# Performance work log

Measured on AMD Instinct MI355X. Metric: run time of the kernel, lower is better.

The kernel has to match this reference:

```python
import jax, jax.numpy as jnp
import numpy as np

B, S, D = 2, 2048, 768
E, L = 4, 2
H = 4 * D  # dim_mlp = dim * mlp_ratio
EPS = 1e-6


def setup_inputs() -> dict:
    key = jax.random.key(0)
    ks = jax.random.split(key, 4)
    x = jax.random.normal(ks[0], (B, S, D), dtype=jnp.float32)
    expert_idx = jax.random.randint(ks[1], (B, S), 0, E, dtype=jnp.int32)
    # Linear weights: normal(std=0.02), biases zero (per init_weights).
    W1 = 0.02 * jax.random.normal(ks[2], (L, E, D, H), dtype=jnp.float32)
    b1 = jnp.zeros((L, E, H), dtype=jnp.float32)
    W2 = 0.02 * jax.random.normal(ks[3], (L, E, H, D), dtype=jnp.float32)
    b2 = jnp.zeros((L, E, D), dtype=jnp.float32)
    # LayerNorm: weight=1, bias=0 (per init_weights).
    ln_g = jnp.ones((L, D), dtype=jnp.float32)
    ln_b = jnp.zeros((L, D), dtype=jnp.float32)
    return {"x": x, "expert_idx": expert_idx, "W1": W1, "b1": b1,
            "W2": W2, "b2": b2, "ln_g": ln_g, "ln_b": ln_b}


def _layernorm(x, g, b):
    mu = jnp.mean(x, axis=-1, keepdims=True)
    var = jnp.mean(jnp.square(x - mu), axis=-1, keepdims=True)
    return (x - mu) * jax.lax.rsqrt(var + EPS) * g + b


def reference(x, expert_idx, W1, b1, W2, b2, ln_g, ln_b):
    # Eval mode: Dropout and DropPath are identity.
    idx = expert_idx[:, :, None, None]  # [B,S,1,1] for gather over expert axis
    for i in range(L):
        h = _layernorm(x, ln_g[i], ln_b[i])                       # [B,S,D]
        # All experts' FFNs computed densely (as in the torch module).
        a = jnp.einsum('bsd,edh->bseh', h, W1[i]) + b1[i]         # [B,S,E,H]
        a = jax.nn.gelu(a, approximate=False)                     # exact GELU (nn.GELU)
        y = jnp.einsum('bseh,ehd->bsed', a, W2[i]) + b2[i]        # [B,S,E,D] == feat_all
        # Per-token gather of the selected expert's slice.
        sel = jnp.take_along_axis(y, idx, axis=2)[:, :, 0, :]     # [B,S,D]
        x = x + sel
    return x
```

## Files before the change

kernel.cpp:

```cpp
#include <hip/hip_runtime.h>
#include <hip/hip_bf16.h>

#define T_TOK 4096
#define DD 768
#define HH 3072
#define EE 4
#define LL 2
#define NELT (T_TOK * DD)

typedef __attribute__((ext_vector_type(8))) short short8;
typedef __attribute__((ext_vector_type(4))) float f32x4;

__device__ __forceinline__ float bf2f(ushort u) { return __uint_as_float(((unsigned)u) << 16); }
__device__ __forceinline__ ushort f2bf(float f) {
  unsigned x = __float_as_uint(f);
  return (ushort)((x + 0x7fffu + ((x >> 16) & 1u)) >> 16);
}

__device__ __forceinline__ void gl2lds16(const void* g, void* l) {
  __builtin_amdgcn_global_load_lds((const __attribute__((address_space(1))) void*)g,
                                   (__attribute__((address_space(3))) void*)l, 16, 0, 0);
}

__global__ __launch_bounds__(256) void prep_kernel(const int* __restrict__ eidx,
                                                   int* __restrict__ inv,
                                                   int* __restrict__ meta) {
  __shared__ int cnt[EE], cur[EE], offs[EE];
  int t = threadIdx.x;
  if (t < EE) { cnt[t] = 0; cur[t] = 0; }
  __syncthreads();
  for (int i = t; i < T_TOK; i += 256) atomicAdd(&cnt[eidx[i]], 1);
  __syncthreads();
  if (t == 0) {
    int off = 0, nt = 0;
    for (int e = 0; e < EE; e++) {
      meta[e] = off; offs[e] = off;
      int c = cnt[e];
      int n = (c + 63) >> 6;
      for (int k = 0; k < n; k++) { meta[8 + nt] = e; meta[96 + nt] = k << 6; nt++; }
      off += c;
    }
    meta[4] = off;
    meta[5] = nt;
  }
  __syncthreads();
  for (int i = t; i < T_TOK; i += 256) {
    int e = eidx[i];
    inv[i] = offs[e] + atomicAdd(&cur[e], 1);
  }
}

template <bool HASY, bool WRITEX>
__global__ __launch_bounds__(256) void ln_kernel(const float* __restrict__ x,
                                                 const float* __restrict__ y,
                                                 const float* __restrict__ g,
                                                 const float* __restrict__ b,
                                                 const int* __restrict__ inv,
                                                 ushort* __restrict__ h,
                                                 float* __restrict__ xf) {
  int wid = blockIdx.x * 4 + (threadIdx.x >> 6);
  int lane = threadIdx.x & 63;
  int pos = inv[wid];
  const float* xr = x + (size_t)wid * DD;
  const float* y0 = y + (size_t)pos * DD;
  const float* y1 = y0 + NELT;
  float v[12], s = 0.f, ss = 0.f;
#pragma unroll
  for (int i = 0; i < 12; i++) {
    int c = lane + i * 64;
    float vv = xr[c];
    if (HASY) vv += y0[c] + y1[c];
    if (WRITEX) xf[(size_t)wid * DD + c] = vv;
    v[i] = vv;
    s += vv; ss += vv * vv;
  }
#pragma unroll
  for (int o = 32; o; o >>= 1) { s += __shfl_xor(s, o, 64); ss += __shfl_xor(ss, o, 64); }
  float mu = s * (1.f / DD);
  float var = ss * (1.f / DD) - mu * mu;
  float rs = rsqrtf(var + 1e-6f);
  ushort* hr = h + (size_t)pos * DD;
#pragma unroll
  for (int i = 0; i < 12; i++) {
    int c = lane + i * 64;
    hr[c] = f2bf((v[i] - mu) * rs * g[c] + b[c]);
  }
}

__global__ __launch_bounds__(256) void store_kernel(const float* __restrict__ xf,
                                                    const float* __restrict__ y,
                                                    const int* __restrict__ inv,
                                                    float* __restrict__ out) {
  int wid = blockIdx.x * 4 + (threadIdx.x >> 6);
  int lane = threadIdx.x & 63;
  int pos = inv[wid];
  const float* xr = xf + (size_t)wid * DD;
  const float* y0 = y + (size_t)pos * DD;
  const float* y1 = y0 + NELT;
  float* o = out + (size_t)wid * DD;
#pragma unroll
  for (int i = 0; i < 12; i++) {
    int c = lane + i * 64;
    o[c] = xr[c] + y0[c] + y1[c];
  }
}

__global__ __launch_bounds__(256) void transpose_f32_bf16(const float* __restrict__ src,
                                                          ushort* __restrict__ dst,
                                                          int R, int C) {
  __shared__ ushort tile[64][68];
  size_t mo = (size_t)blockIdx.z * R * C;
  src += mo;
  dst += mo;
  int c0 = blockIdx.x * 64, r0 = blockIdx.y * 64;
  int t = threadIdx.x;
  int tr = t >> 4;
  int tc = (t & 15) << 2;
#pragma unroll
  for (int i = 0; i < 4; i++) {
    int r = tr + i * 16;
    float4 v = *(const float4*)(src + (size_t)(r0 + r) * C + (c0 + tc));
    tile[r][tc] = f2bf(v.x); tile[r][tc + 1] = f2bf(v.y);
    tile[r][tc + 2] = f2bf(v.z); tile[r][tc + 3] = f2bf(v.w);
  }
  __syncthreads();
#pragma unroll
  for (int i = 0; i < 4; i++) {
    int c = tr + i * 16;
    ushort4 v;
    v.x = tile[tc][c]; v.y = tile[tc + 1][c]; v.z = tile[tc + 2][c]; v.w = tile[tc + 3][c];
    *(ushort4*)(dst + (size_t)(c0 + c) * R + (r0 + tc)) = v;
  }
}

template <int KTOT, int KLEN, int NTOT, bool GELU>
__global__ __launch_bounds__(256, 4) void gemm_kernel(const ushort* __restrict__ A,
                                                      const ushort* __restrict__ Bt,
                                                      const float* __restrict__ bias,
                                                      void* __restrict__ Cout,
                                                      const int* __restrict__ meta) {
  int ty = blockIdx.y;
  if (ty >= meta[5]) return;
  int e = meta[8 + ty];
  int mstart = meta[96 + ty];
  int off0 = meta[e];
  int cnt = meta[e + 1] - off0;
  int ntile = blockIdx.x;
  int z = blockIdx.z;
  int kbegin = z * KLEN;

  __shared__ __align__(16) ushort lds[12288];
  ushort* As = lds;
  ushort* Bs = lds + 4096;

  int tid = threadIdx.x;
  int w = tid >> 6, lane = tid & 63;

  int rr = lane >> 3;
  int swz = ((lane & 7) ^ rr) * 8;
  const ushort* agp[2];
  const ushort* bgp[4];
  ushort* alp[2];
  ushort* blp[4];
#pragma unroll
  for (int i = 0; i < 2; i++) {
    int r = w * 16 + i * 8;
    int arow = off0 + min(mstart + r + rr, cnt - 1);
    agp[i] = A + (size_t)arow * KTOT + kbegin + swz;
    alp[i] = As + r * 64 + lane * 8;
  }
#pragma unroll
  for (int i = 0; i < 4; i++) {
    int r = w * 32 + i * 8;
    int brow = e * NTOT + ntile * 128 + r + rr;
    bgp[i] = Bt + (size_t)brow * KTOT + kbegin + swz;
    blp[i] = Bs + r * 64 + lane * 8;
  }

  int wm = (w >> 1) * 32, wn = (w & 1) * 64;
  int qm = lane & 15;
  int quad = lane >> 4;
  int s7 = qm & 7;

  f32x4 acc[2][4];
#pragma unroll
  for (int mi = 0; mi < 2; mi++)
#pragma unroll
    for (int ni = 0; ni < 4; ni++) acc[mi][ni] = (f32x4){0.f, 0.f, 0.f, 0.f};

  for (int k0 = 0; k0 < KLEN; k0 += 64) {
#pragma unroll
    for (int i = 0; i < 2; i++) gl2lds16(agp[i] + k0, alp[i]);
#pragma unroll
    for (int i = 0; i < 4; i++) gl2lds16(bgp[i] + k0, blp[i]);
    __syncthreads();
#pragma unroll
    for (int h2 = 0; h2 < 2; h2++) {
      int lchunk = ((h2 * 4 + quad) ^ s7) * 8;
      short8 af[2], bfr[4];
#pragma unroll
      for (int mi = 0; mi < 2; mi++)
        af[mi] = *(const short8*)(As + (wm + mi * 16 + qm) * 64 + lchunk);
#pragma unroll
      for (int ni = 0; ni < 4; ni++)
        bfr[ni] = *(const short8*)(Bs + (wn + ni * 16 + qm) * 64 + lchunk);
#pragma unroll
      for (int mi = 0; mi < 2; mi++)
#pragma unroll
        for (int ni = 0; ni < 4; ni++)
          acc[mi][ni] = __builtin_amdgcn_mfma_f32_16x16x32_bf16(af[mi], bfr[ni], acc[mi][ni], 0, 0, 0);
    }
    __syncthreads();
  }

  int rbase = quad * 4;
  float bv[4];
#pragma unroll
  for (int ni = 0; ni < 4; ni++)
    bv[ni] = (!GELU && z != 0) ? 0.f : bias[e * NTOT + ntile * 128 + wn + ni * 16 + qm];

  if (GELU) {
#pragma unroll
    for (int mi = 0; mi < 2; mi++)
#pragma unroll
      for (int ni = 0; ni < 4; ni++) {
        int c = wn + ni * 16 + qm;
#pragma unroll
        for (int r = 0; r < 4; r++) {
          float vv = acc[mi][ni][r] + bv[ni];
          vv = 0.5f * vv * (1.f + erff(vv * 0.70710678118f));
          lds[(wm + mi * 16 + rbase + r) * 128 + c] = f2bf(vv);
        }
      }
    __syncthreads();
    int row0 = tid >> 4;
    int cseg = (tid & 15) * 8;
    ushort* aout = (ushort*)Cout;
#pragma unroll
    for (int it = 0; it < 4; it++) {
      int row = it * 16 + row0;
      int mg = mstart + row;
      if (mg < cnt) {
        short8 v = *(const short8*)(lds + row * 128 + cseg);
        *(short8*)(aout + (size_t)(off0 + mg) * HH + ntile * 128 + cseg) = v;
      }
    }
  } else {
    float* y = (float*)Cout + (size_t)z * NELT;
#pragma unroll
    for (int mi = 0; mi < 2; mi++) {
#pragma unroll
      for (int r = 0; r < 4; r++) {
        int mg = mstart + wm + mi * 16 + rbase + r;
        if (mg >= cnt) continue;
        float* crow = y + (size_t)(off0 + mg) * DD + ntile * 128;
#pragma unroll
        for (int ni = 0; ni < 4; ni++)
          crow[wn + ni * 16 + qm] = acc[mi][ni][r] + bv[ni];
      }
    }
  }
}

extern "C" void kernel_launch(void* const* d_in, const int* in_sizes, int n_in,
                              void* d_out, int out_size, void* d_ws, size_t ws_size,
                              hipStream_t stream) {
  const float* x   = (const float*)d_in[0];
  const int*  eidx = (const int*)d_in[1];
  const float* W1  = (const float*)d_in[2];
  const float* b1  = (const float*)d_in[3];
  const float* W2  = (const float*)d_in[4];
  const float* b2  = (const float*)d_in[5];
  const float* lng = (const float*)d_in[6];
  const float* lnb = (const float*)d_in[7];

  char* ws = (char*)d_ws;
  float*  xf   = (float*)(ws + 0);
  ushort* h    = (ushort*)(ws + 12582912);
  ushort* a    = (ushort*)(ws + 18874368);
  ushort* Wt   = (ushort*)(ws + 44040192);
  float*  y    = (float*)(ws + 62914560);
  int*    inv  = (int*)(ws + 88080384);
  int*    meta = (int*)(ws + 88096768);

  prep_kernel<<<1, 256, 0, stream>>>(eidx, inv, meta);

  for (int l = 0; l < LL; l++) {
    if (l == 0)
      ln_kernel<false, false><<<T_TOK / 4, 256, 0, stream>>>(
          x, y, lng, lnb, inv, h, xf);
    else
      ln_kernel<true, true><<<T_TOK / 4, 256, 0, stream>>>(
          x, y, lng + l * DD, lnb + l * DD, inv, h, xf);
    transpose_f32_bf16<<<dim3(HH / 64, DD / 64, EE), 256, 0, stream>>>(
        W1 + (size_t)l * EE * DD * HH, Wt, DD, HH);
    gemm_kernel<DD, DD, HH, true><<<dim3(HH / 128, 68), 256, 0, stream>>>(
        h, Wt, b1 + l * EE * HH, (void*)a, meta);
    transpose_f32_bf16<<<dim3(DD / 64, HH / 64, EE), 256, 0, stream>>>(
        W2 + (size_t)l * EE * HH * DD, Wt, HH, DD);
    gemm_kernel<HH, HH / 2, DD, false><<<dim3(DD / 128, 68, 2), 256, 0, stream>>>(
        a, Wt, b2 + l * EE * DD, (void*)y, meta);
  }

  store_kernel<<<T_TOK / 4, 256, 0, stream>>>(xf, y, inv, (float*)d_out);
}
```

Measured before the change: 390.7 us.

## Double-buffer LDS tiles in grouped GEMM to overlap global loads with MFMA

Doubles the shared-memory buffer and prefetches the next K-step's A/B tiles via global_load_lds while computing on the current buffer. It uses explicit vmcnt waits and raw barriers instead of two syncthreads per step. The aim is to hide global-memory latency behind MFMA work, at the cost of twice the LDS per block and lower occupancy (launch bounds reduced from 4 to 3 blocks).

```diff
diff --git a/kernel.cpp b/kernel.cpp
--- a/kernel.cpp
+++ b/kernel.cpp
@@ -134,7 +134,7 @@
 }
 
 template <int KTOT, int KLEN, int NTOT, bool GELU>
-__global__ __launch_bounds__(256, 4) void gemm_kernel(const ushort* __restrict__ A,
+__global__ __launch_bounds__(256, 3) void gemm_kernel(const ushort* __restrict__ A,
                                                       const ushort* __restrict__ Bt,
                                                       const float* __restrict__ bias,
                                                       void* __restrict__ Cout,
@@ -149,9 +149,7 @@
   int z = blockIdx.z;
   int kbegin = z * KLEN;
 
-  __shared__ __align__(16) ushort lds[12288];
-  ushort* As = lds;
-  ushort* Bs = lds + 4096;
+  __shared__ __align__(16) ushort lds[24576];
 
   int tid = threadIdx.x;
   int w = tid >> 6, lane = tid & 63;
@@ -160,21 +158,21 @@
   int swz = ((lane & 7) ^ rr) * 8;
   const ushort* agp[2];
   const ushort* bgp[4];
-  ushort* alp[2];
-  ushort* blp[4];
+  int aoff[2];
+  int boff[4];
 #pragma unroll
   for (int i = 0; i < 2; i++) {
     int r = w * 16 + i * 8;
     int arow = off0 + min(mstart + r + rr, cnt - 1);
     agp[i] = A + (size_t)arow * KTOT + kbegin + swz;
-    alp[i] = As + r * 64 + lane * 8;
+    aoff[i] = r * 64 + lane * 8;
   }
 #pragma unroll
   for (int i = 0; i < 4; i++) {
     int r = w * 32 + i * 8;
     int brow = e * NTOT + ntile * 128 + r + rr;
     bgp[i] = Bt + (size_t)brow * KTOT + kbegin + swz;
-    blp[i] = Bs + r * 64 + lane * 8;
+    boff[i] = 4096 + r * 64 + lane * 8;
   }
 
   int wm = (w >> 1) * 32, wn = (w & 1) * 64;
@@ -188,30 +186,54 @@
 #pragma unroll
     for (int ni = 0; ni < 4; ni++) acc[mi][ni] = (f32x4){0.f, 0.f, 0.f, 0.f};
 
-  for (int k0 = 0; k0 < KLEN; k0 += 64) {
-#pragma unroll
-    for (int i = 0; i < 2; i++) gl2lds16(agp[i] + k0, alp[i]);
-#pragma unroll
-    for (int i = 0; i < 4; i++) gl2lds16(bgp[i] + k0, blp[i]);
-    __syncthreads();
+#define STAGE(nb, koff)                                            \
+  do {                                                             \
+    ushort* _b = lds + (nb) * 12288;                               \
+    _Pragma("unroll")                                              \
+    for (int _i = 0; _i < 2; _i++) gl2lds16(agp[_i] + (koff), _b + aoff[_i]); \
+    _Pragma("unroll")                                              \
+    for (int _i = 0; _i < 4; _i++) gl2lds16(bgp[_i] + (koff), _b + boff[_i]); \
+  } while (0)
+
+  constexpr int NSTEPS = KLEN / 64;
+  STAGE(0, 0);
+  asm volatile("" ::: "memory");
+
+#pragma unroll 1
+  for (int s = 0; s < NSTEPS; ++s) {
+    int curb = s & 1;
+    if (s + 1 < NSTEPS) {
+      STAGE(curb ^ 1, (s + 1) * 64);
+      asm volatile("s_waitcnt vmcnt(6)" ::: "memory");
+    } else {
+      asm volatile("s_waitcnt vmcnt(0)" ::: "memory");
+    }
+    __builtin_amdgcn_s_barrier();
+    asm volatile("" ::: "memory");
+
+    const ushort* Asb = lds + curb * 12288;
+    const ushort* Bsb = Asb + 4096;
 #pragma unroll
     for (int h2 = 0; h2 < 2; h2++) {
       int lchunk = ((h2 * 4 + quad) ^ s7) * 8;
       short8 af[2], bfr[4];
 #pragma unroll
       for (int mi = 0; mi < 2; mi++)
-        af[mi] = *(const short8*)(As + (wm + mi * 16 + qm) * 64 + lchunk);
+        af[mi] = *(const short8*)(Asb + (wm + mi * 16 + qm) * 64 + lchunk);
 #pragma unroll
       for (int ni = 0; ni < 4; ni++)
-        bfr[ni] = *(const short8*)(Bs + (wn + ni * 16 + qm) * 64 + lchunk);
+        bfr[ni] = *(const short8*)(Bsb + (wn + ni * 16 + qm) * 64 + lchunk);
 #pragma unroll
       for (int mi = 0; mi < 2; mi++)
 #pragma unroll
         for (int ni = 0; ni < 4; ni++)
           acc[mi][ni] = __builtin_amdgcn_mfma_f32_16x16x32_bf16(af[mi], bfr[ni], acc[mi][ni], 0, 0, 0);
     }
-    __syncthreads();
-  }
+    asm volatile("" ::: "memory");
+    __builtin_amdgcn_s_barrier();
+    asm volatile("" ::: "memory");
+  }
+#undef STAGE
 
   int rbase = quad * 4;
   float bv[4];
```

New measurement: 396.2 us. No clear change (+1.4%).
